# Optimization experiments

Hardware: AMD Instinct MI355X
Metric: run time of the kernel (lower is better)

## Reference

```python
import jax, jax.numpy as jnp
import numpy as np

B, T_RED, C = 16, 512, 512
MAX_DUR = 16


def setup_inputs() -> dict:
    key = jax.random.key(0)
    rng = np.random.default_rng(0)
    durs = np.zeros((B, T_RED), dtype=np.int32)
    for b in range(B):
        nv = int(rng.integers(T_RED // 2, T_RED + 1))
        durs[b, :nv] = rng.integers(1, MAX_DUR + 1, size=nv)
    target_T = durs.sum(axis=1).astype(np.int32)
    pooled_x = jax.random.normal(key, (B, T_RED, C), dtype=jnp.float32)
    return {
        "pooled_x": pooled_x,
        "durations": jnp.asarray(durs),
        "target_T": jnp.asarray(target_T),
    }


def reference(pooled_x, durations, target_T):
    # pooled_x: [B, T_red, C]; durations: [B, T_red] int (0 = pad); target_T: [B]
    Bv, T_red, Cv = pooled_x.shape
    max_len = int(jnp.max(target_T))  # concrete (eager) like the torch .item()

    # torch: valid_durs = durations[b][durations[b] > 0]; feats = pooled_x[b, :num_valid]
    # -> stably compact nonzero durations to the front; pair with leading features.
    order = jnp.argsort(jnp.where(durations > 0, 0, 1), axis=1, stable=True)
    d = jnp.take_along_axis(durations, order, axis=1)            # [B, T_red]
    csum = jnp.cumsum(d, axis=1)                                 # [B, T_red]

    t = jnp.arange(max_len, dtype=csum.dtype)                    # [max_len]
    # repeat_interleave inverse: output frame t belongs to segment
    # s = searchsorted(csum, t, 'right')  (csum[s-1] <= t < csum[s])
    seg = jax.vmap(lambda c: jnp.searchsorted(c, t, side="right"))(csum)  # [B, max_len]
    seg = jnp.minimum(seg, T_red - 1)

    total = csum[:, -1]                                          # len(repeat_interleave result)
    curr_len = jnp.minimum(total, target_T)                      # [B]
    valid = t[None, :] < curr_len[:, None]                       # [B, max_len]

    gathered = jnp.take_along_axis(pooled_x, seg[:, :, None], axis=1)  # [B, max_len, C]
    x_restored = jnp.where(valid[:, :, None], gathered, jnp.zeros((), pooled_x.dtype))
    new_mask = jnp.where(valid, 0, 1).astype(jnp.int32)          # 0 = valid, 1 = padded
    return x_restored, new_mask
```

## Files before the change

### kernel.cpp

```cpp
#include <hip/hip_runtime.h>
#include <hip/hip_bf16.h>

#define B_DIM 16
#define T_RED 512
#define C_DIM 512
#define ROWS_PER_BLK 16

typedef float vfloat4 __attribute__((ext_vector_type(4)));

__device__ inline int block_scan256(int v, int* wsum ) {
    const int lane = threadIdx.x & 63;
    const int wid  = threadIdx.x >> 6;
    int s = v;
    #pragma unroll
    for (int off = 1; off < 64; off <<= 1) {
        int n = __shfl_up(s, off, 64);
        if (lane >= off) s += n;
    }
    if (lane == 63) wsum[wid] = s;
    __syncthreads();
    int add = 0;
    #pragma unroll
    for (int w = 0; w < 4; ++w)
        if (w < wid) add += wsum[w];
    int out = s + add;
    __syncthreads();
    return out;
}

__global__ __launch_bounds__(256) void scatter_fused(
        const vfloat4* __restrict__ x4,
        const int2* __restrict__ dur2,
        vfloat4* __restrict__ out4,
        float* __restrict__ out_mask,
        int max_len) {
    const int b    = blockIdx.y;
    const int base = blockIdx.x * ROWS_PER_BLK;
    const int tid  = threadIdx.x;

    __shared__ int dcomp[T_RED];
    __shared__ int csum[T_RED];
    __shared__ int wsum[4];
    __shared__ int ls[ROWS_PER_BLK];

    const int2 dd = dur2[b * (T_RED / 2) + tid];
    const int d0 = dd.x, d1 = dd.y;
    const int f0 = (d0 > 0) ? 1 : 0;
    const int f1 = (d1 > 0) ? 1 : 0;

    const int S1 = block_scan256(f0 + f1, wsum);
    const int excl = S1 - f0 - f1;
    dcomp[2 * tid]     = 0;
    dcomp[2 * tid + 1] = 0;
    __syncthreads();
    if (f0) dcomp[excl] = d0;
    if (f1) dcomp[excl + f0] = d1;
    __syncthreads();

    const int c0 = dcomp[2 * tid];
    const int c1 = dcomp[2 * tid + 1];
    const int S2 = block_scan256(c0 + c1, wsum);
    csum[2 * tid]     = S2 - c1;
    csum[2 * tid + 1] = S2;
    __syncthreads();

    const int total = csum[T_RED - 1];

    if (tid < ROWS_PER_BLK) {
        const int t = base + tid;
        int src = -1;
        if (t < max_len && t < total) {
            int idx = 0;
            #pragma unroll
            for (int w = 256; w >= 1; w >>= 1) {
                const int cand = idx + w;
                if (cand <= T_RED && csum[cand - 1] <= t) idx = cand;
            }
            const int seg = (idx < T_RED - 1) ? idx : (T_RED - 1);
            src = b * T_RED + seg;
        }
        if (t < max_len) {
            ls[tid] = src;
            out_mask[(size_t)b * max_len + t] = (src >= 0) ? 0.0f : 1.0f;
        }
    }
    __syncthreads();

    const int c4   = tid & 127;
    const int half = tid >> 7;
    #pragma unroll
    for (int p = 0; p < 8; ++p) {
        const int lr = 2 * p + half;
        const int t  = base + lr;
        if (t < max_len) {
            const int s = ls[lr];
            vfloat4 v = (vfloat4)(0.0f);
            if (s >= 0) v = x4[(size_t)s * (C_DIM / 4) + c4];
            __builtin_nontemporal_store(
                v, &out4[((size_t)b * max_len + t) * (C_DIM / 4) + c4]);
        }
    }
}

extern "C" void kernel_launch(void* const* d_in, const int* in_sizes, int n_in,
                              void* d_out, int out_size, void* d_ws, size_t ws_size,
                              hipStream_t stream) {
    const float* pooled_x  = (const float*)d_in[0];
    const int*   durations = (const int*)d_in[1];

    const int max_len = out_size / (B_DIM * (C_DIM + 1));

    float* out_x    = (float*)d_out;
    float* out_mask = out_x + (size_t)B_DIM * max_len * C_DIM;

    dim3 grid((max_len + ROWS_PER_BLK - 1) / ROWS_PER_BLK, B_DIM);
    scatter_fused<<<grid, 256, 0, stream>>>(
        (const vfloat4*)pooled_x, (const int2*)durations,
        (vfloat4*)out_x, out_mask, max_len);
}
```

Measured before the change: 162.1 us.

## Precompute per-frame source index in separate kernel and remap blocks per XCD

Splits the fused kernel in two. A per-batch kernel does the scan once, writes a frame-to-segment index table into workspace, and writes the mask. A gather kernel then reads that table instead of having every block redo two block-wide scans and a binary search. The gather kernel also remaps block IDs so that consecutive work for a batch stays on the same XCD, for L2 locality. The cost is a second launch, a serial build kernel with only 16 blocks that writes the table with scalar loops, and a dependency on workspace being available.

```diff
diff --git a/kernel.cpp b/kernel.cpp
--- a/kernel.cpp
+++ b/kernel.cpp
@@ -1,10 +1,10 @@
 #include <hip/hip_runtime.h>
-#include <hip/hip_bf16.h>
 
 #define B_DIM 16
 #define T_RED 512
 #define C_DIM 512
 #define ROWS_PER_BLK 16
+#define NXCD 8
 
 typedef float vfloat4 __attribute__((ext_vector_type(4)));
 
@@ -26,6 +26,90 @@
     int out = s + add;
     __syncthreads();
     return out;
+}
+
+__global__ __launch_bounds__(256) void build_ls(
+        const int2* __restrict__ dur2,
+        int* __restrict__ ls,
+        float* __restrict__ out_mask,
+        int max_len) {
+    const int b   = blockIdx.x;
+    const int tid = threadIdx.x;
+
+    __shared__ int dcomp[T_RED];
+    __shared__ int wsum[4];
+
+    const int2 dd = dur2[b * (T_RED / 2) + tid];
+    const int d0 = dd.x, d1 = dd.y;
+    const int f0 = (d0 > 0) ? 1 : 0;
+    const int f1 = (d1 > 0) ? 1 : 0;
+
+    const int S1 = block_scan256(f0 + f1, wsum);
+    const int excl = S1 - f0 - f1;
+    dcomp[2 * tid]     = 0;
+    dcomp[2 * tid + 1] = 0;
+    __syncthreads();
+    if (f0) dcomp[excl] = d0;
+    if (f1) dcomp[excl + f0] = d1;
+    __syncthreads();
+
+    const int c0 = dcomp[2 * tid];
+    const int c1 = dcomp[2 * tid + 1];
+    const int S2 = block_scan256(c0 + c1, wsum);
+    const int total = wsum[0] + wsum[1] + wsum[2] + wsum[3];
+
+    int* lsb = ls + (size_t)b * max_len;
+
+    const int st0 = S2 - c1 - c0;
+    for (int k = 0; k < c0; ++k) lsb[st0 + k] = 2 * tid;
+    const int st1 = S2 - c1;
+    for (int k = 0; k < c1; ++k) lsb[st1 + k] = 2 * tid + 1;
+
+    for (int t = total + tid; t < max_len; t += 256) lsb[t] = -1;
+
+    float* mb = out_mask + (size_t)b * max_len;
+    for (int t = tid; t < max_len; t += 256) mb[t] = (t < total) ? 0.0f : 1.0f;
+}
+
+__global__ __launch_bounds__(256) void gather_rows(
+        const vfloat4* __restrict__ x4,
+        const int* __restrict__ ls,
+        vfloat4* __restrict__ out4,
+        int max_len, int blk_per_b) {
+    const int nwg  = gridDim.x;
+    const int orig = blockIdx.x;
+    const int q = nwg / NXCD, r = nwg % NXCD;
+    const int xcd = orig % NXCD, idx = orig / NXCD;
+    const int wg  = (xcd < r ? xcd * (q + 1) : r * (q + 1) + (xcd - r) * q) + idx;
+
+    const int b    = wg / blk_per_b;
+    const int base = (wg % blk_per_b) * ROWS_PER_BLK;
+    const int tid  = threadIdx.x;
+    const int c4   = tid & 127;
+    const int half = tid >> 7;
+
+    const int* lsb = ls + (size_t)b * max_len + base;
+    int srcs[8];
+    #pragma unroll
+    for (int p = 0; p < 8; ++p) {
+        const int t = base + 2 * p + half;
+        srcs[p] = (t < max_len) ? lsb[2 * p + half] : -1;
+    }
+
+    const vfloat4* xb = x4 + (size_t)b * T_RED * (C_DIM / 4);
+    vfloat4* ob = out4 + ((size_t)b * max_len + base) * (C_DIM / 4);
+
+    #pragma unroll
+    for (int p = 0; p < 8; ++p) {
+        const int t = base + 2 * p + half;
+        if (t < max_len) {
+            vfloat4 v = (vfloat4)(0.0f);
+            const int s = srcs[p];
+            if (s >= 0) v = xb[(size_t)s * (C_DIM / 4) + c4];
+            __builtin_nontemporal_store(
+                v, &ob[(size_t)(2 * p + half) * (C_DIM / 4) + c4]);
+        }
+    }
 }
 
 __global__ __launch_bounds__(256) void scatter_fused(
@@ -113,8 +197,20 @@
     float* out_x    = (float*)d_out;
     float* out_mask = out_x + (size_t)B_DIM * max_len * C_DIM;
 
-    dim3 grid((max_len + ROWS_PER_BLK - 1) / ROWS_PER_BLK, B_DIM);
-    scatter_fused<<<grid, 256, 0, stream>>>(
-        (const vfloat4*)pooled_x, (const int2*)durations,
-        (vfloat4*)out_x, out_mask, max_len);
-}
+    const size_t ls_bytes = (size_t)B_DIM * max_len * sizeof(int);
+
+    if (d_ws != nullptr && ws_size >= ls_bytes) {
+        int* ls = (int*)d_ws;
+        build_ls<<<dim3(B_DIM), dim3(256), 0, stream>>>(
+            (const int2*)durations, ls, out_mask, max_len);
+
+        const int blk_per_b = (max_len + ROWS_PER_BLK - 1) / ROWS_PER_BLK;
+        gather_rows<<<dim3(blk_per_b * B_DIM), dim3(256), 0, stream>>>(
+            (const vfloat4*)pooled_x, ls, (vfloat4*)out_x, max_len, blk_per_b);
+    } else {
+        dim3 grid((max_len + ROWS_PER_BLK - 1) / ROWS_PER_BLK, B_DIM);
+        scatter_fused<<<grid, dim3(256), 0, stream>>>(
+            (const vfloat4*)pooled_x, (const int2*)durations,
+            (vfloat4*)out_x, out_mask, max_len);
+    }
+}
```

Measured after the change: 168.1 us. 3.7% more time.
